# Kernel optimization log

Hardware: AMD Instinct MI355X
Metric: run time of the kernel (lower is better)

Reference implementation:

```python
import jax, jax.numpy as jnp
import numpy as np

IN, H, B, T = 64, 256, 128, 512

def _uniform(key, shape, std):
    return jax.random.uniform(key, shape, jnp.float32, -std, std)

def setup_inputs() -> dict:
    key = jax.random.key(0)
    ks = jax.random.split(key, 16)
    std = 1.0 / np.sqrt(H)
    inp = {
        'x': jax.random.normal(ks[0], (B, T, IN), jnp.float32),
        # layer 1 sLSTM cell
        'Wxh1': _uniform(ks[1], (4 * H, IN), std), 'bxh1': _uniform(ks[2], (4 * H,), std),
        'Whh1': _uniform(ks[3], (4 * H, H), std),  'bhh1': _uniform(ks[4], (4 * H,), std),
        # layer 2 sLSTM cell
        'Wxh2': _uniform(ks[5], (4 * H, H), std),  'bxh2': _uniform(ks[6], (4 * H,), std),
        'Whh2': _uniform(ks[7], (4 * H, H), std),  'bhh2': _uniform(ks[8], (4 * H,), std),
        # head MLP
        'W1': _uniform(ks[9], (H // 2, H), 1.0 / np.sqrt(H)),      'b1': _uniform(ks[10], (H // 2,), 1.0 / np.sqrt(H)),
        'W2': _uniform(ks[11], (H // 4, H // 2), 1.0 / np.sqrt(H // 2)), 'b2': _uniform(ks[12], (H // 4,), 1.0 / np.sqrt(H // 2)),
        'W3': _uniform(ks[13], (1, H // 4), 1.0 / np.sqrt(H // 4)),      'b3': _uniform(ks[14], (1,), 1.0 / np.sqrt(H // 4)),
    }
    return inp

def _slstm_cell(x, h, c, m, n, Wxh, bxh, Whh, bhh):
    # gates: [B, 4H]
    gates = x @ Wxh.T + bxh + h @ Whh.T + bhh
    ig, fg, zg, og = jnp.split(gates, 4, axis=1)
    z_t = jnp.tanh(zg)
    o_t = jax.nn.sigmoid(og)
    # stabilizer: log(exp(fg)) = fg, log(exp(ig)) = ig
    m_t = jnp.maximum(fg + m, ig)
    i_t = jnp.exp(ig - m_t)
    f_t = jnp.exp(fg + m - m_t)
    c_t = f_t * c + i_t * z_t
    n_t = f_t * n + i_t
    h_t = o_t * (c_t / n_t)
    return h_t, c_t, m_t, n_t

def reference(x, Wxh1, bxh1, Whh1, bhh1, Wxh2, bxh2, Whh2, bhh2, W1, b1, W2, b2, W3, b3):
    Bq = x.shape[0]
    z = jnp.zeros((Bq, H), x.dtype)
    init = (z, z, z, z, z, z, z, z)  # (h1,c1,m1,n1,h2,c2,m2,n2)

    def step(carry, x_t):
        h1, c1, m1, n1, h2, c2, m2, n2 = carry
        h1, c1, m1, n1 = _slstm_cell(x_t, h1, c1, m1, n1, Wxh1, bxh1, Whh1, bhh1)
        h2, c2, m2, n2 = _slstm_cell(h1, h2, c2, m2, n2, Wxh2, bxh2, Whh2, bhh2)
        return (h1, c1, m1, n1, h2, c2, m2, n2), None

    carry, _ = jax.lax.scan(step, init, jnp.swapaxes(x, 0, 1))  # scan over time
    out = carry[4]  # last h2 == outputs[:, -1, :]
    out = jax.nn.relu(out @ W1.T + b1)   # dropout is identity in eval
    out = jax.nn.relu(out @ W2.T + b2)
    out = out @ W3.T + b3
    return out.squeeze(-1)  # [B]
```

## Files before the change

### kernel.cpp

```cpp
#include <hip/hip_runtime.h>
#include <stdint.h>

typedef unsigned short ushort_t;
typedef __attribute__((ext_vector_type(8))) short short8;
typedef __attribute__((ext_vector_type(4))) float float4v;
typedef __attribute__((ext_vector_type(4))) int int4v;

#define TSTEPS 512
#define NBATCH 128
#define HID 256
#define NIN 64
#define RB 32
#define NBHID (NBATCH*HID)

#define OFF_FLAGS   0u
#define OFF_BIAS    16384u
#define OFF_H1R     32768u
#define RING_BYTES  (RB*(unsigned)NBATCH*HID*4u)
#define OFF_H2R     (OFF_H1R + RING_BYTES)
#define OFF_WF1     (OFF_H2R + RING_BYTES)
#define WF1_FRAGS   (16*8*4*4)
#define OFF_WF2     (OFF_WF1 + WF1_FRAGS*1024u)
#define WF2_FRAGS   (16*8*6*4)
#define OFF_HOUT    (OFF_WF2 + WF2_FRAGS*1024u)


__device__ __forceinline__ ushort_t bf16h(float f) {
    unsigned u = __float_as_uint(f);
    u += 0x7fffu + ((u >> 16) & 1u);
    return (ushort_t)(u >> 16);
}
__device__ __forceinline__ float bf16f(ushort_t h) {
    return __uint_as_float(((unsigned)h) << 16);
}


__device__ __forceinline__ int ld_cg_i32(const void* p) {
    int r;
    asm volatile("global_load_dword %0, %1, off sc0 sc1\n\ts_waitcnt vmcnt(0)"
                 : "=v"(r) : "v"(p) : "memory");
    return r;
}
__device__ __forceinline__ float ld_cg_f32(const void* p) {
    float r;
    asm volatile("global_load_dword %0, %1, off sc0 sc1\n\ts_waitcnt vmcnt(0)"
                 : "=v"(r) : "v"(p) : "memory");
    return r;
}
__device__ __forceinline__ void ld2x4(int4v& a, int4v& b, const void* p) {
    asm volatile("global_load_dwordx4 %0, %2, off sc0 sc1\n\t"
                 "global_load_dwordx4 %1, %2, off offset:16 sc0 sc1\n\t"
                 "s_waitcnt vmcnt(0)"
                 : "=&v"(a), "=&v"(b) : "v"(p) : "memory");
}
__device__ __forceinline__ void ld4x4(int4v& a, int4v& b, int4v& c, int4v& d,
                                      const void* p, const void* q) {
    asm volatile("global_load_dwordx4 %0, %4, off sc0 sc1\n\t"
                 "global_load_dwordx4 %1, %4, off offset:16 sc0 sc1\n\t"
                 "global_load_dwordx4 %2, %5, off sc0 sc1\n\t"
                 "global_load_dwordx4 %3, %5, off offset:16 sc0 sc1\n\t"
                 "s_waitcnt vmcnt(0)"
                 : "=&v"(a), "=&v"(b), "=&v"(c), "=&v"(d)
                 : "v"(p), "v"(q) : "memory");
}
__device__ __forceinline__ void st_cg_u32(void* p, unsigned v) {
    asm volatile("global_store_dword %0, %1, off sc0 sc1" :: "v"(p), "v"(v) : "memory");
}
__device__ __forceinline__ void st_cg_f32(void* p, float v) {
    asm volatile("global_store_dword %0, %1, off sc0 sc1" :: "v"(p), "v"(v) : "memory");
}
__device__ __forceinline__ void flag_release(int* p, int v) {
    asm volatile("s_waitcnt vmcnt(0)\n\tglobal_store_dword %0, %1, off sc0 sc1"
                 :: "v"(p), "v"(v) : "memory");
}

__device__ __forceinline__ int4v ext_hi8(int4v a, int4v b) {
    int4v r;
    r[0] = (int)__builtin_amdgcn_perm((unsigned)a[1], (unsigned)a[0], 0x05040100u);
    r[1] = (int)__builtin_amdgcn_perm((unsigned)a[3], (unsigned)a[2], 0x05040100u);
    r[2] = (int)__builtin_amdgcn_perm((unsigned)b[1], (unsigned)b[0], 0x05040100u);
    r[3] = (int)__builtin_amdgcn_perm((unsigned)b[3], (unsigned)b[2], 0x05040100u);
    return r;
}
__device__ __forceinline__ int4v ext_lo8(int4v a, int4v b) {
    int4v r;
    r[0] = (int)__builtin_amdgcn_perm((unsigned)a[1], (unsigned)a[0], 0x07060302u);
    r[1] = (int)__builtin_amdgcn_perm((unsigned)a[3], (unsigned)a[2], 0x07060302u);
    r[2] = (int)__builtin_amdgcn_perm((unsigned)b[1], (unsigned)b[0], 0x07060302u);
    r[3] = (int)__builtin_amdgcn_perm((unsigned)b[3], (unsigned)b[2], 0x07060302u);
    return r;
}


__global__ void prep_misc(const float* bxh1, const float* bhh1,
                          const float* bxh2, const float* bhh2,
                          float* bias, int* flags, unsigned* h1r, unsigned* h2r)
{
    int n = blockIdx.x * blockDim.x + threadIdx.x;
    if (n < 1024)       bias[n] = bxh1[n] + bhh1[n];
    else if (n < 2048)  bias[n] = bxh2[n - 1024] + bhh2[n - 1024];
    else if (n < 6144)  flags[n - 2048] = 0;
    else {
        int d = n - 6144;
        if (d < 2 * NBHID) {
            unsigned* ring = (d < NBHID) ? h1r : h2r;
            int e = (d < NBHID) ? d : d - NBHID;
            ring[(size_t)(RB - 1) * NBHID + e] = 0u;
        }
    }
}

__global__ void prep_wf(const float* Wxh1, const float* Whh1,
                        const float* Wxh2, const float* Whh2,
                        ushort_t* wf1, ushort_t* wf2)
{
    int n = blockIdx.x * blockDim.x + threadIdx.x;
    const int L1E = WF1_FRAGS * 512;
    const int L2E = WF2_FRAGS * 512;
    if (n >= L1E + L2E) return;
    int layer = (n >= L1E) ? 1 : 0;
    int e = layer ? (n - L1E) : n;
    int el = e & 511;
    int f  = e >> 9;
    int lane = el >> 3, j = el & 7;
    int nt = f & 3;
    int rem = f >> 2;
    int i, wv, slice, F, S;
    if (!layer) { F = 4; S = 10; i = rem & 3; wv = (rem >> 2) & 7; slice = rem >> 5; }
    else        { F = 6; S = 16; i = rem % 6; int r2 = rem / 6; wv = r2 & 7; slice = r2 >> 3; }
    int fg = wv * F + i;
    int col = lane & 15;
    int row = nt * 256 + slice * 16 + col;
    float val = 0.f;
    if (fg < 3 * S) {
        int sec = (fg < S) ? 0 : ((fg < 2 * S) ? 1 : 2);
        int ks = (fg - sec * S) * 32 + (lane >> 4) * 8 + j;
        float w;
        if (!layer) w = (ks < 256) ? Whh1[row * 256 + ks] : Wxh1[row * 64 + (ks - 256)];
        else        w = (ks < 256) ? Wxh2[row * 256 + ks] : Whh2[row * 256 + (ks - 256)];
        ushort_t hi = bf16h(w);
        val = (sec < 2) ? bf16f(hi) : (w - bf16f(hi));
    }
    (layer ? wf2 : wf1)[e] = bf16h(val);
}


template<int LAYER, int F, int S, int PITCH>
__device__ __forceinline__ void run_layer(
    int g, int slice, int tid, const float* __restrict__ x,
    int* flags, const float* bias,
    unsigned* h1r, unsigned* h2r, const ushort_t* wfrag, float* hOut,
    ushort_t* sA, ushort_t* sB, float (*red)[4][64][4])
{
    const int wv = tid >> 6, lane = tid & 63;
    const int mrow = lane & 15, q = lane >> 4;
    int* f1 = flags + g * 256;
    int* f2 = flags + 2048 + g * 256;
    int* myflag = flags + LAYER * 2048 + g * 256 + slice * 16;

    short8 bw[4][F];
    {
        const ushort_t* base = wfrag + (size_t)((slice * 8 + wv) * F) * 4 * 512;
        #pragma unroll
        for (int i = 0; i < F; i++)
            #pragma unroll
            for (int nt = 0; nt < 4; nt++)
                bw[nt][i] = *(const short8*)(base + (i * 4 + nt) * 512 + lane * 8);
    }

    float bs[4];
    #pragma unroll
    for (int nt = 0; nt < 4; nt++)
        bs[nt] = bias[LAYER * 1024 + nt * 256 + slice * 16 + mrow];

    float cst[4] = {0,0,0,0}, mst[4] = {0,0,0,0}, nst[4] = {0,0,0,0};

    const int sr = tid >> 5, k = tid & 31;
    const int row = g * 16 + sr;

    for (int t = 0; t < TSTEPS; t++) {
        if (LAYER == 0 && tid >= 128 && tid < 256) {
            int idx = tid - 128;
            int r = idx >> 3, o = idx & 7;
            const float* xsrc = x + ((size_t)(g * 16 + r) * TSTEPS + t) * NIN + o * 8;
            float4v x0 = *(const float4v*)xsrc;
            float4v x1 = *(const float4v*)(xsrc + 4);
            float xs[8] = {x0[0], x0[1], x0[2], x0[3], x1[0], x1[1], x1[2], x1[3]};
            union { ushort_t u[8]; int4v v4; } hiP, loP;
            #pragma unroll
            for (int z = 0; z < 8; z++) {
                ushort_t hi = bf16h(xs[z]);
                hiP.u[z] = hi;
                loP.u[z] = bf16h(xs[z] - bf16f(hi));
            }
            *(int4v*)(sA + r * PITCH + (32 + o) * 8) = hiP.v4;
            *(int4v*)(sB + r * PITCH + (32 + o) * 8) = loP.v4;
        }

        if (tid >= 64 && tid < 128) {
            int pl = tid - 64;
            int* p = nullptr; int thr = 0;
            if (LAYER == 0) {
                if (pl < 16)      { p = f1 + pl * 16;        thr = t; }
                else if (pl < 32) { p = f2 + (pl - 16) * 16; thr = t - 30; }
            } else {
                if (pl < 16)      { p = f1 + pl * 16;        thr = t + 1; }
                else if (pl < 32) { p = f2 + (pl - 16) * 16; thr = t; }
            }
            if (p)
                while (ld_cg_i32(p) < thr) { }
        }
        __syncthreads();

        {
            if (LAYER == 0) {
                const unsigned* base = h1r + ((size_t)((t - 1) & (RB - 1)) * NBATCH + row) * HID + k * 8;
                int4v a, b;
                ld2x4(a, b, base);
                *(int4v*)(sA + sr * PITCH + k * 8) = ext_hi8(a, b);
                *(int4v*)(sB + sr * PITCH + k * 8) = ext_lo8(a, b);
            } else {
                const unsigned* b1 = h1r + ((size_t)(t & (RB - 1)) * NBATCH + row) * HID + k * 8;
                const unsigned* b2 = h2r + ((size_t)((t - 1) & (RB - 1)) * NBATCH + row) * HID + k * 8;
                int4v a, b, c, d;
                ld4x4(a, b, c, d, b1, b2);
                *(int4v*)(sA + sr * PITCH + k * 8)        = ext_hi8(a, b);
                *(int4v*)(sB + sr * PITCH + k * 8)        = ext_lo8(a, b);
                *(int4v*)(sA + sr * PITCH + (32 + k) * 8) = ext_hi8(c, d);
                *(int4v*)(sB + sr * PITCH + (32 + k) * 8) = ext_lo8(c, d);
            }
        }
        __syncthreads();

        float4v acc[4] = {};
        #pragma unroll
        for (int i = 0; i < F; i++) {
            const int fg = wv * F + i;
            short8 a;
            if (fg < 3 * S) {
                int sec = (fg >= S && fg < 2 * S) ? 1 : 0;
                int ks = ((fg < S) ? fg : ((fg < 2 * S) ? fg - S : fg - 2 * S)) * 32;
                const ushort_t* ap = (sec ? sB : sA) + mrow * PITCH + ks + q * 8;
                a = *(const short8*)ap;
            } else {
                a = (short8){0,0,0,0,0,0,0,0};
            }
            #pragma unroll
            for (int nt = 0; nt < 4; nt++)
                acc[nt] = __builtin_amdgcn_mfma_f32_16x16x32_bf16(a, bw[nt][i], acc[nt], 0, 0, 0);
        }

        if (wv >= 4) {
            #pragma unroll
            for (int nt = 0; nt < 4; nt++) *(float4v*)red[wv][nt][lane] = acc[nt];
        }
        __syncthreads();
        if (wv < 4) {
            #pragma unroll
            for (int nt = 0; nt < 4; nt++) acc[nt] += *(const float4v*)red[wv + 4][nt][lane];
            if (wv >= 2) {
                #pragma unroll
                for (int nt = 0; nt < 4; nt++) *(float4v*)red[wv][nt][lane] = acc[nt];
            }
        }
        __syncthreads();
        if (wv < 2) {
            #pragma unroll
            for (int nt = 0; nt < 4; nt++) acc[nt] += *(const float4v*)red[wv + 2][nt][lane];
            if (wv == 1) {
                #pragma unroll
                for (int nt = 0; nt < 4; nt++) *(float4v*)red[1][nt][lane] = acc[nt];
            }
        }
        __syncthreads();

        if (wv == 0) {
            #pragma unroll
            for (int nt = 0; nt < 4; nt++) acc[nt] += *(const float4v*)red[1][nt][lane];

            unsigned* ring = LAYER ? h2r : h1r;
            unsigned* base = ring + (size_t)(t & (RB - 1)) * NBHID;
            #pragma unroll
            for (int r2 = 0; r2 < 4; r2++) {
                float ig  = acc[0][r2] + bs[0];
                float fgt = acc[1][r2] + bs[1];
                float zg  = acc[2][r2] + bs[2];
                float og  = acc[3][r2] + bs[3];
                float zc = fminf(fmaxf(zg, -15.f), 15.f);
                float e2 = __expf(2.f * zc);
                float zt = (e2 - 1.f) / (e2 + 1.f);
                float ot = 1.f / (1.f + __expf(-og));
                float mt = fmaxf(fgt + mst[r2], ig);
                float it = __expf(ig - mt);
                float ft = __expf(fgt + mst[r2] - mt);
                cst[r2] = ft * cst[r2] + it * zt;
                nst[r2] = ft * nst[r2] + it;
                mst[r2] = mt;
                float h = ot * (cst[r2] / nst[r2]);
                ushort_t hi = bf16h(h);
                ushort_t lo = bf16h(h - bf16f(hi));
                int orow = g * 16 + q * 4 + r2;
                int col = slice * 16 + mrow;
                st_cg_u32(base + (size_t)orow * HID + col, ((unsigned)lo << 16) | (unsigned)hi);
                if (LAYER == 1 && t == TSTEPS - 1)
                    st_cg_f32(hOut + (size_t)orow * HID + col, h);
            }
            if (lane == 0)
                flag_release(myflag, t + 1);
        }
    }
}

__global__ __launch_bounds__(512, 2) void recur(
    const float* __restrict__ x,
    int* flags, const float* bias,
    unsigned* h1r, unsigned* h2r, const ushort_t* wf1, const ushort_t* wf2, float* hOut)
{
    __shared__ alignas(16) ushort_t sA[16 * 520];
    __shared__ alignas(16) ushort_t sB[16 * 520];
    __shared__ float red[8][4][64][4];
    int g = blockIdx.x & 7;
    int loc = blockIdx.x >> 3;
    if (loc < 16)
        run_layer<0, 4, 10, 328>(g, loc, threadIdx.x, x, flags, bias, h1r, h2r, wf1, hOut, sA, sB, red);
    else
        run_layer<1, 6, 16, 520>(g, loc - 16, threadIdx.x, x, flags, bias, h1r, h2r, wf2, hOut, sA, sB, red);
}


__global__ void head_mlp(const float* hOut, const float* W1, const float* b1,
                         const float* W2, const float* b2, const float* W3, const float* b3,
                         float* out)
{
    __shared__ float h[256];
    __shared__ float a1[128];
    __shared__ float a2[64];
    int b = blockIdx.x, j = threadIdx.x;
    for (int k = j; k < 256; k += 128)
        h[k] = ld_cg_f32(hOut + (size_t)b * HID + k);
    __syncthreads();
    float s = b1[j];
    for (int k = 0; k < 256; k++) s += W1[j * 256 + k] * h[k];
    a1[j] = fmaxf(s, 0.f);
    __syncthreads();
    if (j < 64) {
        float s2 = b2[j];
        for (int k = 0; k < 128; k++) s2 += W2[j * 128 + k] * a1[k];
        a2[j] = fmaxf(s2, 0.f);
    }
    __syncthreads();
    if (j == 0) {
        float s3 = b3[0];
        for (int k = 0; k < 64; k++) s3 += W3[k] * a2[k];
        out[b] = s3;
    }
}


extern "C" void kernel_launch(void* const* d_in, const int* in_sizes, int n_in,
                              void* d_out, int out_size, void* d_ws, size_t ws_size,
                              hipStream_t stream)
{
    const float* x    = (const float*)d_in[0];
    const float* Wxh1 = (const float*)d_in[1];
    const float* bxh1 = (const float*)d_in[2];
    const float* Whh1 = (const float*)d_in[3];
    const float* bhh1 = (const float*)d_in[4];
    const float* Wxh2 = (const float*)d_in[5];
    const float* bxh2 = (const float*)d_in[6];
    const float* Whh2 = (const float*)d_in[7];
    const float* bhh2 = (const float*)d_in[8];
    const float* W1   = (const float*)d_in[9];
    const float* b1   = (const float*)d_in[10];
    const float* W2   = (const float*)d_in[11];
    const float* b2   = (const float*)d_in[12];
    const float* W3   = (const float*)d_in[13];
    const float* b3   = (const float*)d_in[14];

    char* w = (char*)d_ws;
    int*      flags = (int*)(w + OFF_FLAGS);
    float*    bias  = (float*)(w + OFF_BIAS);
    unsigned* h1r   = (unsigned*)(w + OFF_H1R);
    unsigned* h2r   = (unsigned*)(w + OFF_H2R);
    ushort_t* wf1   = (ushort_t*)(w + OFF_WF1);
    ushort_t* wf2   = (ushort_t*)(w + OFF_WF2);
    float*    hOut  = (float*)(w + OFF_HOUT);

    prep_misc<<<(6144 + 2 * NBHID + 255) / 256, 256, 0, stream>>>(
        bxh1, bhh1, bxh2, bhh2, bias, flags, h1r, h2r);
    prep_wf<<<((WF1_FRAGS + WF2_FRAGS) * 512 + 255) / 256, 256, 0, stream>>>(
        Wxh1, Whh1, Wxh2, Whh2, wf1, wf2);

    const float* xp = x;
    void* args[] = { (void*)&xp, (void*)&flags, (void*)&bias,
                     (void*)&h1r, (void*)&h2r, (void*)&wf1, (void*)&wf2, (void*)&hOut };
    hipLaunchCooperativeKernel((void*)recur, dim3(256), dim3(512), args, 0, stream);

    head_mlp<<<NBATCH, 128, 0, stream>>>(hOut, W1, b1, W2, b2, W3, b3, (float*)d_out);
}
```

Measured before the change: 2.009 ms.

## Embed generation tag bits in ring data to replace per-step flag handshakes

Each step's producer now stores a generation bit in the LSB of the bf16 hi half of every ring element. Consumers spin on the data itself, both on one sentinel element and on every loaded vector, so the per-step flag store and its vmcnt wait go away. Ring-reuse flags are now written and checked only every 8 steps. The 4-stage tree reduction across waves is replaced by a single-barrier reduction into wave 0. The tag bit slightly perturbs the hi mantissa, which the lo residual compensates. The whole ring must now be initialised with tag 1, which adds work to the prep kernel.

```diff
diff --git a/kernel.cpp b/kernel.cpp
--- a/kernel.cpp
+++ b/kernel.cpp
@@ -12,6 +12,7 @@
 #define NIN 64
 #define RB 32
 #define NBHID (NBATCH*HID)
+#define RING_DW (RB*NBHID)
 
 #define OFF_FLAGS   0u
 #define OFF_BIAS    16384u
@@ -33,6 +34,9 @@
 __device__ __forceinline__ float bf16f(ushort_t h) {
     return __uint_as_float(((unsigned)h) << 16);
 }
+__device__ __forceinline__ unsigned genbit(int s) {
+    return ((unsigned)(s + 64) >> 5) & 1u;
+}
 
 
 __device__ __forceinline__ int ld_cg_i32(const void* p) {
@@ -66,12 +70,19 @@
 __device__ __forceinline__ void st_cg_u32(void* p, unsigned v) {
     asm volatile("global_store_dword %0, %1, off sc0 sc1" :: "v"(p), "v"(v) : "memory");
 }
+__device__ __forceinline__ void st_cg_i32(int* p, int v) {
+    asm volatile("global_store_dword %0, %1, off sc0 sc1" :: "v"(p), "v"(v) : "memory");
+}
 __device__ __forceinline__ void st_cg_f32(void* p, float v) {
     asm volatile("global_store_dword %0, %1, off sc0 sc1" :: "v"(p), "v"(v) : "memory");
 }
-__device__ __forceinline__ void flag_release(int* p, int v) {
-    asm volatile("s_waitcnt vmcnt(0)\n\tglobal_store_dword %0, %1, off sc0 sc1"
-                 :: "v"(p), "v"(v) : "memory");
+
+__device__ __forceinline__ bool tag8(int4v a, int4v b, unsigned gw) {
+    unsigned x = ((unsigned)a[0] ^ gw) | ((unsigned)a[1] ^ gw) |
+                 ((unsigned)a[2] ^ gw) | ((unsigned)a[3] ^ gw) |
+                 ((unsigned)b[0] ^ gw) | ((unsigned)b[1] ^ gw) |
+                 ((unsigned)b[2] ^ gw) | ((unsigned)b[3] ^ gw);
+    return (x & 1u) == 0u;
 }
 
 __device__ __forceinline__ int4v ext_hi8(int4v a, int4v b) {
@@ -94,19 +105,16 @@
 
 __global__ void prep_misc(const float* bxh1, const float* bhh1,
                           const float* bxh2, const float* bhh2,
-                          float* bias, int* flags, unsigned* h1r, unsigned* h2r)
+                          float* bias, int* flags, unsigned* ring_all)
 {
     int n = blockIdx.x * blockDim.x + threadIdx.x;
     if (n < 1024)       bias[n] = bxh1[n] + bhh1[n];
     else if (n < 2048)  bias[n] = bxh2[n - 1024] + bhh2[n - 1024];
     else if (n < 6144)  flags[n - 2048] = 0;
     else {
-        int d = n - 6144;
-        if (d < 2 * NBHID) {
-            unsigned* ring = (d < NBHID) ? h1r : h2r;
-            int e = (d < NBHID) ? d : d - NBHID;
-            ring[(size_t)(RB - 1) * NBHID + e] = 0u;
-        }
+        unsigned d = n - 6144;
+        if (d < 2u * RING_DW)
+            ring_all[d] = 0x00000001u;
     }
 }
 
@@ -199,31 +207,55 @@
 
         if (tid >= 64 && tid < 128) {
             int pl = tid - 64;
-            int* p = nullptr; int thr = 0;
-            if (LAYER == 0) {
-                if (pl < 16)      { p = f1 + pl * 16;        thr = t; }
-                else if (pl < 32) { p = f2 + (pl - 16) * 16; thr = t - 30; }
-            } else {
-                if (pl < 16)      { p = f1 + pl * 16;        thr = t + 1; }
-                else if (pl < 32) { p = f2 + (pl - 16) * 16; thr = t; }
+            if (pl < 16) {
+                const unsigned* sp;
+                unsigned want;
+                if (LAYER == 0) {
+                    sp = h1r + (size_t)((t - 1) & (RB - 1)) * NBHID
+                             + (size_t)(g * 16 + 15) * HID + pl * 16 + 15;
+                    want = genbit(t - 1);
+                } else {
+                    sp = h1r + (size_t)(t & (RB - 1)) * NBHID
+                             + (size_t)(g * 16 + 15) * HID + pl * 16 + 15;
+                    want = genbit(t);
+                }
+                while ((((unsigned)ld_cg_i32(sp)) & 1u) != want) { }
+            } else if (pl < 32) {
+                if (LAYER == 1) {
+                    const unsigned* sp = h2r + (size_t)((t - 1) & (RB - 1)) * NBHID
+                                             + (size_t)(g * 16 + 15) * HID + (pl - 16) * 16 + 15;
+                    unsigned want = genbit(t - 1);
+                    while ((((unsigned)ld_cg_i32(sp)) & 1u) != want) { }
+                }
+            } else if ((t & 7) == 0) {
+                int thr = t - 22;
+                const int* p = nullptr;
+                if (LAYER == 0) {
+                    if (pl < 48)      p = f1 + (pl - 32) * 16;
+                    else              p = f2 + (pl - 48) * 16;
+                } else {
+                    if (pl < 48)      p = f2 + (pl - 32) * 16;
+                }
+                if (p)
+                    while (ld_cg_i32(p) < thr) { }
             }
-            if (p)
-                while (ld_cg_i32(p) < thr) { }
         }
         __syncthreads();
 
         {
             if (LAYER == 0) {
                 const unsigned* base = h1r + ((size_t)((t - 1) & (RB - 1)) * NBATCH + row) * HID + k * 8;
+                unsigned w = genbit(t - 1);
                 int4v a, b;
-                ld2x4(a, b, base);
+                do { ld2x4(a, b, base); } while (!tag8(a, b, w));
                 *(int4v*)(sA + sr * PITCH + k * 8) = ext_hi8(a, b);
                 *(int4v*)(sB + sr * PITCH + k * 8) = ext_lo8(a, b);
             } else {
                 const unsigned* b1 = h1r + ((size_t)(t & (RB - 1)) * NBATCH + row) * HID + k * 8;
                 const unsigned* b2 = h2r + ((size_t)((t - 1) & (RB - 1)) * NBATCH + row) * HID + k * 8;
+                unsigned w1 = genbit(t), w2 = genbit(t - 1);
                 int4v a, b, c, d;
-                ld4x4(a, b, c, d, b1, b2);
+                do { ld4x4(a, b, c, d, b1, b2); } while (!(tag8(a, b, w1) && tag8(c, d, w2)));
                 *(int4v*)(sA + sr * PITCH + k * 8)        = ext_hi8(a, b);
                 *(int4v*)(sB + sr * PITCH + k * 8)        = ext_lo8(a, b);
                 *(int4v*)(sA + sr * PITCH + (32 + k) * 8) = ext_hi8(c, d);
@@ -231,6 +263,9 @@
             }
         }
         __syncthreads();
+
+        if (tid == 256 && (t & 7) == 0)
+            st_cg_i32(myflag, t);
 
         float4v acc[4] = {};
         #pragma unroll
@@ -250,36 +285,22 @@
                 acc[nt] = __builtin_amdgcn_mfma_f32_16x16x32_bf16(a, bw[nt][i], acc[nt], 0, 0, 0);
         }
 
-        if (wv >= 4) {
-            #pragma unroll
-            for (int nt = 0; nt < 4; nt++) *(float4v*)red[wv][nt][lane] = acc[nt];
+        if (wv != 0) {
+            #pragma unroll
+            for (int nt = 0; nt < 4; nt++) *(float4v*)red[wv - 1][nt][lane] = acc[nt];
         }
         __syncthreads();
-        if (wv < 4) {
-            #pragma unroll
-            for (int nt = 0; nt < 4; nt++) acc[nt] += *(const float4v*)red[wv + 4][nt][lane];
-            if (wv >= 2) {
+
+        if (wv == 0) {
+            #pragma unroll
+            for (int w = 0; w < 7; w++)
                 #pragma unroll
-                for (int nt = 0; nt < 4; nt++) *(float4v*)red[wv][nt][lane] = acc[nt];
-            }
-        }
-        __syncthreads();
-        if (wv < 2) {
-            #pragma unroll
-            for (int nt = 0; nt < 4; nt++) acc[nt] += *(const float4v*)red[wv + 2][nt][lane];
-            if (wv == 1) {
-                #pragma unroll
-                for (int nt = 0; nt < 4; nt++) *(float4v*)red[1][nt][lane] = acc[nt];
-            }
-        }
-        __syncthreads();
-
-        if (wv == 0) {
-            #pragma unroll
-            for (int nt = 0; nt < 4; nt++) acc[nt] += *(const float4v*)red[1][nt][lane];
+                for (int nt = 0; nt < 4; nt++)
+                    acc[nt] += *(const float4v*)red[w][nt][lane];
 
             unsigned* ring = LAYER ? h2r : h1r;
             unsigned* base = ring + (size_t)(t & (RB - 1)) * NBHID;
+            unsigned gw = genbit(t);
             #pragma unroll
             for (int r2 = 0; r2 < 4; r2++) {
                 float ig  = acc[0][r2] + bs[0];
@@ -297,16 +318,15 @@
                 nst[r2] = ft * nst[r2] + it;
                 mst[r2] = mt;
                 float h = ot * (cst[r2] / nst[r2]);
-                ushort_t hi = bf16h(h);
-                ushort_t lo = bf16h(h - bf16f(hi));
+                ushort_t hi = (ushort_t)(((unsigned)bf16h(h) & 0xFFFEu) | gw);
+                float rem = h - bf16f(hi);
+                ushort_t lo = bf16h(rem);
                 int orow = g * 16 + q * 4 + r2;
                 int col = slice * 16 + mrow;
                 st_cg_u32(base + (size_t)orow * HID + col, ((unsigned)lo << 16) | (unsigned)hi);
                 if (LAYER == 1 && t == TSTEPS - 1)
                     st_cg_f32(hOut + (size_t)orow * HID + col, h);
             }
-            if (lane == 0)
-                flag_release(myflag, t + 1);
         }
     }
 }
@@ -318,7 +338,7 @@
 {
     __shared__ alignas(16) ushort_t sA[16 * 520];
     __shared__ alignas(16) ushort_t sB[16 * 520];
-    __shared__ float red[8][4][64][4];
+    __shared__ float red[7][4][64][4];
     int g = blockIdx.x & 7;
     int loc = blockIdx.x >> 3;
     if (loc < 16)
@@ -386,8 +406,8 @@
     ushort_t* wf2   = (ushort_t*)(w + OFF_WF2);
     float*    hOut  = (float*)(w + OFF_HOUT);
 
-    prep_misc<<<(6144 + 2 * NBHID + 255) / 256, 256, 0, stream>>>(
-        bxh1, bhh1, bxh2, bhh2, bias, flags, h1r, h2r);
+    prep_misc<<<(6144 + 2 * RING_DW + 255) / 256, 256, 0, stream>>>(
+        bxh1, bhh1, bxh2, bhh2, bias, flags, h1r);
     prep_wf<<<((WF1_FRAGS + WF2_FRAGS) * 512 + 255) / 256, 256, 0, stream>>>(
         Wxh1, Whh1, Wxh2, Whh2, wf1, wf2);
 
```

After: 1.863 ms. -7.3%, faster.
